# Optimization experiments

Measured on AMD Instinct MI355X. Metric: run time of the kernel, lower is better.

The kernel has to match this reference:

```python
import jax, jax.numpy as jnp
import numpy as np

N_NODES = 100000
N_EDGES = 1600000
IN_C, HID, OUT_C = 16, 64, 1


def setup_inputs() -> dict:
    key = jax.random.key(0)
    ks = jax.random.split(key, 12)
    x = jax.random.normal(ks[0], (N_NODES, IN_C), dtype=jnp.float32)
    edge_index = jax.random.randint(ks[1], (2, N_EDGES), 0, N_NODES, dtype=jnp.int32)

    def lin(k, fan_in, fan_out):
        s = 1.0 / np.sqrt(fan_in)
        kw, kb = jax.random.split(k)
        W = jax.random.uniform(kw, (fan_in, fan_out), jnp.float32, -s, s)
        b = jax.random.uniform(kb, (fan_out,), jnp.float32, -s, s)
        return W, b

    W0, b0 = lin(ks[2], IN_C, HID)      # node_mlps[0]
    W1, b1 = lin(ks[3], HID, HID)       # node_mlps[1]
    W2, b2 = lin(ks[4], HID, OUT_C)     # node_mlps[2]
    M0, bM0 = lin(ks[5], 2 * HID, HID)  # message_mlps[0] (only one used for num_layers=3)
    return {"x": x, "edge_index": edge_index, "W0": W0, "b0": b0,
            "W1": W1, "b1": b1, "W2": W2, "b2": b2, "M0": M0, "bM0": bM0}


def _message_passing(h, src, dst, M, bM):
    # gather -> concat -> linear -> scatter-add -> degree normalize
    msgs = jnp.concatenate([h[src], h[dst]], axis=1) @ M + bM  # [E, HID]
    agg = jax.ops.segment_sum(msgs, dst, num_segments=N_NODES)  # [N, HID]
    deg = jax.ops.segment_sum(jnp.ones((src.shape[0],), h.dtype), dst,
                              num_segments=N_NODES)
    deg = jnp.clip(deg, 1.0, None)[:, None]
    return agg / deg


def reference(x, edge_index, W0, b0, W1, b1, W2, b2, M0, bM0):
    src, dst = edge_index[0], edge_index[1]
    h = jax.nn.relu(x @ W0 + b0)                  # node_mlps[0] (dropout = eval identity)
    h = h + _message_passing(h, src, dst, M0, bM0)
    h = jax.nn.relu(h @ W1 + b1)                  # node_mlps[1]
    return h @ W2 + b2                            # node_mlps[2], [N, 1]
```

## Files before the change

### kernel.cpp

```cpp
#include <hip/hip_runtime.h>

#define HID 64
#define IN_C 16

typedef __attribute__((ext_vector_type(8))) short short8;
typedef __attribute__((ext_vector_type(4))) float f32x4;

__device__ __forceinline__ float bitsf(unsigned u) { return __uint_as_float(u); }
__device__ __forceinline__ float lanebcf(float v, int l) {
    return __int_as_float(__builtin_amdgcn_readlane(__float_as_int(v), l));
}
__device__ __forceinline__ float f4c(const float4& a, int c) {
    switch (c & 3) { case 0: return a.x; case 1: return a.y; case 2: return a.z; default: return a.w; }
}

__global__ void k_init(const float* __restrict__ M0, const float* __restrict__ W1,
                       const float* __restrict__ bM0, const float* __restrict__ b1,
                       ushort* __restrict__ WPhi, ushort* __restrict__ WPlo,
                       float* __restrict__ bias192) {
    int tid = blockIdx.x * 256 + threadIdx.x;
    if (tid >= 64 * 192) return;
    int cc = tid % 192;
    int k  = tid / 192;
    float w;
    if (cc < 64) {
        float a = 0.f;
#pragma unroll
        for (int m = 0; m < HID; ++m) a = fmaf(M0[k * HID + m], W1[m * HID + cc], a);
        w = a;
    } else if (cc < 128) {
        int c = cc - 64;
        float a = W1[k * HID + c];
#pragma unroll
        for (int m = 0; m < HID; ++m) a = fmaf(M0[(HID + k) * HID + m], W1[m * HID + c], a);
        w = a;
    } else {
        w = W1[k * HID + (cc - 128)];
    }
    unsigned wb = __float_as_uint(w);
    ushort hi = (ushort)(wb >> 16);
    float hif = __uint_as_float(wb & 0xffff0000u);
    ushort lo = (ushort)(__float_as_uint(w - hif) >> 16);
    int ct = cc >> 4, s = k >> 5, l = ((k >> 3) & 3) * 16 + (cc & 15), j = k & 7;
    int fi = ((ct * 2 + s) * 64 + l) * 8 + j;
    WPhi[fi] = hi;
    WPlo[fi] = lo;
    if (k == 0) {
        float bv;
        if (cc < 64) bv = 0.f;
        else if (cc < 128) {
            int c = cc - 64;
            float a = b1[c];
#pragma unroll
            for (int m = 0; m < HID; ++m) a = fmaf(bM0[m], W1[m * HID + c], a);
            bv = a;
        } else bv = b1[cc - 128];
        bias192[cc] = bv;
    }
}

__global__ __launch_bounds__(256) void k_pre(
    const float* __restrict__ x, const float* __restrict__ W0, const float* __restrict__ b0,
    const ushort* __restrict__ WPhi, const ushort* __restrict__ WPlo,
    const float* __restrict__ bias192,
    ushort* __restrict__ zb, float* __restrict__ PQ, float* __restrict__ Pp, int N)
{
    __shared__ ushort hhi[64 * 64];
    __shared__ ushort hlo[64 * 64];

    int tid  = threadIdx.x;
    int lane = tid & 63;
    int w    = tid >> 6;
    int n0   = blockIdx.x * 64;

    float w0c[IN_C];
#pragma unroll
    for (int k = 0; k < IN_C; ++k) w0c[k] = W0[k * HID + lane];
    float b0l = b0[lane];

    short8 Bhi[3][2], Blo[3][2];
    float bias[3];
#pragma unroll
    for (int i = 0; i < 3; ++i) {
        int ct = w * 3 + i;
#pragma unroll
        for (int s = 0; s < 2; ++s) {
            int fi = ((ct * 2 + s) * 64 + lane) * 8;
            Bhi[i][s] = *reinterpret_cast<const short8*>(WPhi + fi);
            Blo[i][s] = *reinterpret_cast<const short8*>(WPlo + fi);
        }
        bias[i] = bias192[ct * 16 + (lane & 15)];
    }

    int nx = n0 + w * 16 + (lane >> 2);
    float4 xq = make_float4(0.f, 0.f, 0.f, 0.f);
    if (nx < N) xq = *reinterpret_cast<const float4*>(x + (size_t)nx * IN_C + (lane & 3) * 4);

#pragma unroll
    for (int nn = 0; nn < 16; ++nn) {
        float acc = b0l;
#pragma unroll
        for (int k = 0; k < IN_C; ++k)
            acc = fmaf(lanebcf(f4c(xq, k & 3), 4 * nn + (k >> 2)), w0c[k], acc);
        float h = fmaxf(acc, 0.f);
        unsigned hb = __float_as_uint(h);
        ushort hi = (ushort)(hb >> 16);
        float hif = __uint_as_float(hb & 0xffff0000u);
        ushort lo = (ushort)(__float_as_uint(h - hif) >> 16);
        int nl = w * 16 + nn;
        int u  = ((lane >> 3) ^ (nl & 7));
        int off = nl * 64 + u * 8 + (lane & 7);
        hhi[off] = hi;
        hlo[off] = lo;
    }
    __syncthreads();

#pragma unroll
    for (int st = 0; st < 4; ++st) {
        int nloc = st * 16 + (lane & 15);
        short8 Ahi[2], Alo[2];
#pragma unroll
        for (int s = 0; s < 2; ++s) {
            int u = (s * 4 + (lane >> 4)) ^ (nloc & 7);
            int off = nloc * 64 + u * 8;
            Ahi[s] = *reinterpret_cast<const short8*>(hhi + off);
            Alo[s] = *reinterpret_cast<const short8*>(hlo + off);
        }
#pragma unroll
        for (int i = 0; i < 3; ++i) {
            int ct = w * 3 + i;
            f32x4 acc = {bias[i], bias[i], bias[i], bias[i]};
#pragma unroll
            for (int s = 0; s < 2; ++s) {
                acc = __builtin_amdgcn_mfma_f32_16x16x32_bf16(Ahi[s], Bhi[i][s], acc, 0, 0, 0);
                acc = __builtin_amdgcn_mfma_f32_16x16x32_bf16(Ahi[s], Blo[i][s], acc, 0, 0, 0);
                acc = __builtin_amdgcn_mfma_f32_16x16x32_bf16(Alo[s], Bhi[i][s], acc, 0, 0, 0);
                acc = __builtin_amdgcn_mfma_f32_16x16x32_bf16(Alo[s], Blo[i][s], acc, 0, 0, 0);
            }
            int ch = ct * 16 + (lane & 15);
#pragma unroll
            for (int r = 0; r < 4; ++r) {
                int n = n0 + st * 16 + (lane >> 4) * 4 + r;
                if (n >= N) continue;
                float v = acc[r];
                if (ch < 64) {
                    unsigned u = __float_as_uint(v);
                    unsigned rr = (u + 0x7fffu + ((u >> 16) & 1u)) >> 16;
                    zb[(size_t)n * HID + ch] = (ushort)rr;
                } else if (ch < 128) {
                    PQ[(size_t)n * HID + (ch - 64)] = v;
                } else {
                    Pp[(size_t)n * HID + (ch - 128)] = v;
                }
            }
        }
    }
}

__global__ __launch_bounds__(256) void k_p1hist(const int* __restrict__ ei, int* __restrict__ bhT,
                                                int E, int B1) {
    __shared__ int h[1024];
    int NB1 = gridDim.x;
    for (int i = threadIdx.x; i < B1; i += 256) h[i] = 0;
    __syncthreads();
    int CH = (E + NB1 - 1) / NB1;
    int e0 = blockIdx.x * CH;
    int e1 = min(e0 + CH, E);
    for (int e = e0 + (int)threadIdx.x; e < e1; e += 256)
        atomicAdd(&h[ei[E + e] >> 8], 1);
    __syncthreads();
    for (int i = threadIdx.x; i < B1; i += 256)
        bhT[(size_t)i * NB1 + blockIdx.x] = h[i];
}

__global__ void k_scan1(const int* __restrict__ cnt, int* __restrict__ rs,
                        int* __restrict__ bsum, int M) {
    __shared__ int lds[256];
    int t = threadIdx.x;
    int base = blockIdx.x * 4096 + t * 16;
    int v[16];
    if (base + 16 <= M) {
#pragma unroll
        for (int u = 0; u < 4; ++u) {
            int4 w = *reinterpret_cast<const int4*>(cnt + base + u * 4);
            v[u * 4 + 0] = w.x; v[u * 4 + 1] = w.y; v[u * 4 + 2] = w.z; v[u * 4 + 3] = w.w;
        }
    } else {
#pragma unroll
        for (int u = 0; u < 16; ++u) v[u] = (base + u < M) ? cnt[base + u] : 0;
    }
    int run = 0;
#pragma unroll
    for (int u = 0; u < 16; ++u) { int tv = v[u]; v[u] = run; run += tv; }
    lds[t] = run;
    __syncthreads();
#pragma unroll
    for (int off = 1; off < 256; off <<= 1) {
        int xw = (t >= off) ? lds[t - off] : 0;
        __syncthreads();
        lds[t] += xw;
        __syncthreads();
    }
    int excl = lds[t] - run;
    if (t == 255) bsum[blockIdx.x] = lds[255];
#pragma unroll
    for (int u = 0; u < 16; ++u)
        if (base + u < M) rs[base + u] = excl + v[u];
}

__global__ void k_scan_add(int* __restrict__ rs, const int* __restrict__ bsum,
                           int NB, int M, int E) {
    __shared__ int lds[256];
    __shared__ int excl[256];
    int t = threadIdx.x;
    int v = (t < NB) ? bsum[t] : 0;
    lds[t] = v;
    __syncthreads();
#pragma unroll
    for (int off = 1; off < 256; off <<= 1) {
        int xw = (t >= off) ? lds[t - off] : 0;
        __syncthreads();
        lds[t] += xw;
        __syncthreads();
    }
    excl[t] = lds[t] - v;
    __syncthreads();
    int i = blockIdx.x * 256 + t;
    if (i < M) rs[i] += excl[i >> 12];
    if (i == 0) rs[M] = E;
}

__global__ __launch_bounds__(256) void k_p1scat(const int* __restrict__ ei, const int* __restrict__ off,
                                                int2* __restrict__ tmp, int E, int B1) {
    __shared__ int cur[1024];
    int NB1 = gridDim.x;
    for (int i = threadIdx.x; i < B1; i += 256)
        cur[i] = off[(size_t)i * NB1 + blockIdx.x];
    __syncthreads();
    int CH = (E + NB1 - 1) / NB1;
    int e0 = blockIdx.x * CH;
    int e1 = min(e0 + CH, E);
    for (int e = e0 + (int)threadIdx.x; e < e1; e += 256) {
        int s = ei[e];
        int d = ei[E + e];
        int pos = atomicAdd(&cur[d >> 8], 1);
        tmp[pos] = make_int2(s, d);
    }
}

__global__ __launch_bounds__(256) void k_p2(const int2* __restrict__ tmp, const int* __restrict__ off,
                                            int* __restrict__ rs, int* __restrict__ csr,
                                            int E, int N, int B1, int NB1) {
    __shared__ int h2[256];
    __shared__ int sc[256];
    __shared__ int cur[256];
    int b = blockIdx.x;
    int t = threadIdx.x;
    int bb0 = off[(size_t)b * NB1];
    int bb1 = off[(size_t)(b + 1) * NB1];

    h2[t] = 0;
    __syncthreads();
    for (int i = bb0 + t; i < bb1; i += 256)
        atomicAdd(&h2[tmp[i].y & 255], 1);
    __syncthreads();

    int v = h2[t];
    sc[t] = v;
    __syncthreads();
#pragma unroll
    for (int o = 1; o < 256; o <<= 1) {
        int xw = (t >= o) ? sc[t - o] : 0;
        __syncthreads();
        sc[t] += xw;
        __syncthreads();
    }
    int excl = sc[t] - v;

    int node = b * 256 + t;
    if (node < N) rs[node] = bb0 + excl;
    if (b == B1 - 1 && t == 0) rs[N] = E;
    cur[t] = bb0 + excl;
    __syncthreads();

    for (int i = bb0 + t; i < bb1; i += 256) {
        int2 ed = tmp[i];
        int pos = atomicAdd(&cur[ed.y & 255], 1);
        csr[pos] = ed.x;
    }
}

__global__ __launch_bounds__(256) void k_final(
    const ushort* __restrict__ zb, const float* __restrict__ PQ, const float* __restrict__ Pp,
    const int* __restrict__ rs, const int* __restrict__ csr,
    const float* __restrict__ W2, const float* __restrict__ b2,
    float* __restrict__ out, int N)
{
    int lane = threadIdx.x & 63;
    int g    = lane >> 4;
    int ql   = lane & 15;
    int oct  = ql & 7;
    int half = ql >> 3;
    int wid  = (blockIdx.x * 256 + threadIdx.x) >> 6;
    int nw   = (gridDim.x * 256) >> 6;

    int c0 = oct * 8 + half * 4;
    float4 w2v = *reinterpret_cast<const float4*>(W2 + c0);
    float b2s = b2[0];

    for (int n0 = wid * 4; n0 < N; n0 += nw * 4) {
        int ng   = n0 + g;
        bool okg = ng < N;

        int rv = okg ? rs[ng + half] : 0;
        int beg = __shfl(rv, g * 16 + 0);
        int end = __shfl(rv, g * 16 + 8);
        int deg = end - beg;
        int md = deg;
        md = max(md, __shfl_xor(md, 16));
        md = max(md, __shfl_xor(md, 32));

        float acc[8];
#pragma unroll
        for (int i = 0; i < 8; ++i) acc[i] = 0.f;

        for (int c = 0; c < md; c += 32) {
            int j0 = c + ql, j1 = c + 16 + ql;
            int ia = (j0 < deg) ? csr[beg + j0] : -1;
            int ib = (j1 < deg) ? csr[beg + j1] : -1;
#pragma unroll
            for (int tb = 0; tb < 4; ++tb) {
                if (tb > 0 && md <= c + 8 * tb) break;
                int srcs[4];
#pragma unroll
                for (int t4 = 0; t4 < 4; ++t4) {
                    int t = tb * 4 + t4;
                    int e = 2 * t + half;
                    srcs[t4] = __shfl(tb < 2 ? ia : ib, g * 16 + (e & 15));
                }
                uint4 rw[4];
#pragma unroll
                for (int t4 = 0; t4 < 4; ++t4) {
                    int s = srcs[t4] < 0 ? 0 : srcs[t4];
                    rw[t4] = *reinterpret_cast<const uint4*>(zb + (size_t)s * HID + oct * 8);
                }
#pragma unroll
                for (int t4 = 0; t4 < 4; ++t4) {
                    if (srcs[t4] >= 0) {
                        uint4 wv = rw[t4];
                        acc[0] += bitsf(wv.x << 16); acc[1] += bitsf(wv.x & 0xffff0000u);
                        acc[2] += bitsf(wv.y << 16); acc[3] += bitsf(wv.y & 0xffff0000u);
                        acc[4] += bitsf(wv.z << 16); acc[5] += bitsf(wv.z & 0xffff0000u);
                        acc[6] += bitsf(wv.w << 16); acc[7] += bitsf(wv.w & 0xffff0000u);
                    }
                }
            }
        }
#pragma unroll
        for (int i = 0; i < 8; ++i) acc[i] += __shfl_xor(acc[i], 8);

        float s0 = half ? acc[4] : acc[0];
        float s1 = half ? acc[5] : acc[1];
        float s2 = half ? acc[6] : acc[2];
        float s3 = half ? acc[7] : acc[3];

        float4 base = make_float4(0.f, 0.f, 0.f, 0.f);
        if (okg) {
            base = *reinterpret_cast<const float4*>(PQ + (size_t)ng * HID + c0);
            if (deg == 0)
                base = *reinterpret_cast<const float4*>(Pp + (size_t)ng * HID + c0);
        }
        float rcpd = (deg > 0) ? (1.f / (float)deg) : 0.f;
        float y0 = base.x + s0 * rcpd;
        float y1 = base.y + s1 * rcpd;
        float y2 = base.z + s2 * rcpd;
        float y3 = base.w + s3 * rcpd;

        float part = fmaxf(y0, 0.f) * w2v.x + fmaxf(y1, 0.f) * w2v.y +
                     fmaxf(y2, 0.f) * w2v.z + fmaxf(y3, 0.f) * w2v.w;
#pragma unroll
        for (int off = 1; off < 16; off <<= 1) part += __shfl_xor(part, off);
        if (ql == 0 && okg) out[ng] = part + b2s;
    }
}

extern "C" void kernel_launch(void* const* d_in, const int* in_sizes, int n_in,
                              void* d_out, int out_size, void* d_ws, size_t ws_size,
                              hipStream_t stream) {
    const float* x   = (const float*)d_in[0];
    const int*   ei  = (const int*)d_in[1];
    const float* W0  = (const float*)d_in[2];
    const float* b0  = (const float*)d_in[3];
    const float* W1  = (const float*)d_in[4];
    const float* b1  = (const float*)d_in[5];
    const float* W2  = (const float*)d_in[6];
    const float* b2  = (const float*)d_in[7];
    const float* M0  = (const float*)d_in[8];
    const float* bM0 = (const float*)d_in[9];

    int N = in_sizes[0] / IN_C;
    int E = in_sizes[1] / 2;
    int B1 = (N + 255) >> 8;
    int NB1 = 256;
    int M2 = B1 * NB1;
    int NB = (M2 + 4095) / 4096;

    ushort* zb     = (ushort*)d_ws;
    float*  PQ     = (float*)(zb + (size_t)N * HID);
    float*  Pp     = PQ + (size_t)N * HID;
    ushort* WPhi   = (ushort*)(Pp + (size_t)N * HID);
    ushort* WPlo   = WPhi + 12288;
    float*  bias192= (float*)(WPlo + 12288);
    int*    bhT    = (int*)(bias192 + 192);
    int*    off    = bhT + (size_t)M2;
    int*    bsum   = off + (size_t)M2 + 1;
    int*    rs     = bsum + 256;
    size_t  up     = ((size_t)(rs + N + 1) + 7) & ~(size_t)7;
    int2*   tmp    = (int2*)up;
    int*    csr    = (int*)(tmp + (size_t)E);
    float*  out    = (float*)d_out;

    int npre = (N + 63) / 64;

    k_init<<<48, 256, 0, stream>>>(M0, W1, bM0, b1, WPhi, WPlo, bias192);
    k_pre<<<npre, 256, 0, stream>>>(x, W0, b0, WPhi, WPlo, bias192, zb, PQ, Pp, N);
    k_p1hist<<<NB1, 256, 0, stream>>>(ei, bhT, E, B1);
    k_scan1<<<NB, 256, 0, stream>>>(bhT, off, bsum, M2);
    k_scan_add<<<(M2 + 255) / 256, 256, 0, stream>>>(off, bsum, NB, M2, E);
    k_p1scat<<<NB1, 256, 0, stream>>>(ei, off, tmp, E, B1);
    k_p2<<<B1, 256, 0, stream>>>(tmp, off, rs, csr, E, N, B1, NB1);
    k_final<<<2048, 256, 0, stream>>>(zb, PQ, Pp, rs, csr, W2, b2, out, N);
}
```

Baseline: 112.2 us.

## Fuse edge histogram into pre kernel, vectorize outputs, pack sort temp

Merges the edge-destination histogram kernel into the node pre-processing launch as extra blocks, which removes one launch and lets both workloads overlap. It swaps the MFMA operand order so each lane holds four consecutive channels of one node, so results are written as packed bf16x4 or float4 stores instead of scattered scalar stores. It also packs the source index and low destination byte into one 32-bit word in the two-pass sort temp buffer, halving that traffic. The packing assumes source indices fit in 24 bits.

New measurement: 101.7 us. 9.3% less time.

```diff
diff --git a/kernel.cpp b/kernel.cpp
--- a/kernel.cpp
+++ b/kernel.cpp
@@ -7,6 +7,10 @@
 typedef __attribute__((ext_vector_type(4))) float f32x4;
 
 __device__ __forceinline__ float bitsf(unsigned u) { return __uint_as_float(u); }
+__device__ __forceinline__ unsigned rne16(float f) {
+    unsigned u = __float_as_uint(f);
+    return (u + 0x7fffu + ((u >> 16) & 1u)) >> 16;
+}
 __device__ __forceinline__ float lanebcf(float v, int l) {
     return __int_as_float(__builtin_amdgcn_readlane(__float_as_int(v), l));
 }
@@ -59,37 +63,53 @@
     }
 }
 
-__global__ __launch_bounds__(256) void k_pre(
+__global__ __launch_bounds__(256) void k_pre_hist(
     const float* __restrict__ x, const float* __restrict__ W0, const float* __restrict__ b0,
     const ushort* __restrict__ WPhi, const ushort* __restrict__ WPlo,
     const float* __restrict__ bias192,
-    ushort* __restrict__ zb, float* __restrict__ PQ, float* __restrict__ Pp, int N)
+    ushort* __restrict__ zb, float* __restrict__ PQ, float* __restrict__ Pp, int N,
+    const int* __restrict__ ei, int* __restrict__ bhT, int E, int B1, int NB1)
 {
     __shared__ ushort hhi[64 * 64];
     __shared__ ushort hlo[64 * 64];
 
+    if ((int)blockIdx.x < NB1) {
+        int* h = reinterpret_cast<int*>(hhi);
+        for (int i = threadIdx.x; i < B1; i += 256) h[i] = 0;
+        __syncthreads();
+        int CH = (E + NB1 - 1) / NB1;
+        int e0 = blockIdx.x * CH;
+        int e1 = min(e0 + CH, E);
+        for (int e = e0 + (int)threadIdx.x; e < e1; e += 256)
+            atomicAdd(&h[ei[E + e] >> 8], 1);
+        __syncthreads();
+        for (int i = threadIdx.x; i < B1; i += 256)
+            bhT[(size_t)i * NB1 + blockIdx.x] = h[i];
+        return;
+    }
+
     int tid  = threadIdx.x;
     int lane = tid & 63;
     int w    = tid >> 6;
-    int n0   = blockIdx.x * 64;
+    int n0   = (blockIdx.x - NB1) * 64;
 
     float w0c[IN_C];
 #pragma unroll
     for (int k = 0; k < IN_C; ++k) w0c[k] = W0[k * HID + lane];
     float b0l = b0[lane];
 
-    short8 Bhi[3][2], Blo[3][2];
-    float bias[3];
+    short8 Whi[3][2], Wlo[3][2];
+    float4 bias4[3];
 #pragma unroll
     for (int i = 0; i < 3; ++i) {
         int ct = w * 3 + i;
 #pragma unroll
         for (int s = 0; s < 2; ++s) {
             int fi = ((ct * 2 + s) * 64 + lane) * 8;
-            Bhi[i][s] = *reinterpret_cast<const short8*>(WPhi + fi);
-            Blo[i][s] = *reinterpret_cast<const short8*>(WPlo + fi);
-        }
-        bias[i] = bias192[ct * 16 + (lane & 15)];
+            Whi[i][s] = *reinterpret_cast<const short8*>(WPhi + fi);
+            Wlo[i][s] = *reinterpret_cast<const short8*>(WPlo + fi);
+        }
+        bias4[i] = *reinterpret_cast<const float4*>(bias192 + ct * 16 + (lane >> 4) * 4);
     }
 
     int nx = n0 + w * 16 + (lane >> 2);
@@ -126,51 +146,35 @@
             Ahi[s] = *reinterpret_cast<const short8*>(hhi + off);
             Alo[s] = *reinterpret_cast<const short8*>(hlo + off);
         }
+        int n = n0 + st * 16 + (lane & 15);
 #pragma unroll
         for (int i = 0; i < 3; ++i) {
             int ct = w * 3 + i;
-            f32x4 acc = {bias[i], bias[i], bias[i], bias[i]};
+            f32x4 acc = {bias4[i].x, bias4[i].y, bias4[i].z, bias4[i].w};
 #pragma unroll
             for (int s = 0; s < 2; ++s) {
-                acc = __builtin_amdgcn_mfma_f32_16x16x32_bf16(Ahi[s], Bhi[i][s], acc, 0, 0, 0);
-                acc = __builtin_amdgcn_mfma_f32_16x16x32_bf16(Ahi[s], Blo[i][s], acc, 0, 0, 0);
-                acc = __builtin_amdgcn_mfma_f32_16x16x32_bf16(Alo[s], Bhi[i][s], acc, 0, 0, 0);
-                acc = __builtin_amdgcn_mfma_f32_16x16x32_bf16(Alo[s], Blo[i][s], acc, 0, 0, 0);
+                acc = __builtin_amdgcn_mfma_f32_16x16x32_bf16(Whi[i][s], Ahi[s], acc, 0, 0, 0);
+                acc = __builtin_amdgcn_mfma_f32_16x16x32_bf16(Whi[i][s], Alo[s], acc, 0, 0, 0);
+                acc = __builtin_amdgcn_mfma_f32_16x16x32_bf16(Wlo[i][s], Ahi[s], acc, 0, 0, 0);
+                acc = __builtin_amdgcn_mfma_f32_16x16x32_bf16(Wlo[i][s], Alo[s], acc, 0, 0, 0);
             }
-            int ch = ct * 16 + (lane & 15);
-#pragma unroll
-            for (int r = 0; r < 4; ++r) {
-                int n = n0 + st * 16 + (lane >> 4) * 4 + r;
-                if (n >= N) continue;
-                float v = acc[r];
-                if (ch < 64) {
-                    unsigned u = __float_as_uint(v);
-                    unsigned rr = (u + 0x7fffu + ((u >> 16) & 1u)) >> 16;
-                    zb[(size_t)n * HID + ch] = (ushort)rr;
-                } else if (ch < 128) {
-                    PQ[(size_t)n * HID + (ch - 64)] = v;
+            if (n < N) {
+                int chb = ct * 16 + (lane >> 4) * 4;
+                if (chb < 64) {
+                    uint2 pk;
+                    pk.x = rne16(acc[0]) | (rne16(acc[1]) << 16);
+                    pk.y = rne16(acc[2]) | (rne16(acc[3]) << 16);
+                    *reinterpret_cast<uint2*>(zb + (size_t)n * HID + chb) = pk;
+                } else if (chb < 128) {
+                    float4 v = make_float4(acc[0], acc[1], acc[2], acc[3]);
+                    *reinterpret_cast<float4*>(PQ + (size_t)n * HID + (chb - 64)) = v;
                 } else {
-                    Pp[(size_t)n * HID + (ch - 128)] = v;
+                    float4 v = make_float4(acc[0], acc[1], acc[2], acc[3]);
+                    *reinterpret_cast<float4*>(Pp + (size_t)n * HID + (chb - 128)) = v;
                 }
             }
         }
     }
-}
-
-__global__ __launch_bounds__(256) void k_p1hist(const int* __restrict__ ei, int* __restrict__ bhT,
-                                                int E, int B1) {
-    __shared__ int h[1024];
-    int NB1 = gridDim.x;
-    for (int i = threadIdx.x; i < B1; i += 256) h[i] = 0;
-    __syncthreads();
-    int CH = (E + NB1 - 1) / NB1;
-    int e0 = blockIdx.x * CH;
-    int e1 = min(e0 + CH, E);
-    for (int e = e0 + (int)threadIdx.x; e < e1; e += 256)
-        atomicAdd(&h[ei[E + e] >> 8], 1);
-    __syncthreads();
-    for (int i = threadIdx.x; i < B1; i += 256)
-        bhT[(size_t)i * NB1 + blockIdx.x] = h[i];
 }
 
 __global__ void k_scan1(const int* __restrict__ cnt, int* __restrict__ rs,
@@ -231,7 +235,7 @@
 }
 
 __global__ __launch_bounds__(256) void k_p1scat(const int* __restrict__ ei, const int* __restrict__ off,
-                                                int2* __restrict__ tmp, int E, int B1) {
+                                                unsigned* __restrict__ tmp, int E, int B1) {
     __shared__ int cur[1024];
     int NB1 = gridDim.x;
     for (int i = threadIdx.x; i < B1; i += 256)
@@ -244,11 +248,11 @@
         int s = ei[e];
         int d = ei[E + e];
         int pos = atomicAdd(&cur[d >> 8], 1);
-        tmp[pos] = make_int2(s, d);
-    }
-}
-
-__global__ __launch_bounds__(256) void k_p2(const int2* __restrict__ tmp, const int* __restrict__ off,
+        tmp[pos] = (unsigned)s | ((unsigned)(d & 255) << 24);
+    }
+}
+
+__global__ __launch_bounds__(256) void k_p2(const unsigned* __restrict__ tmp, const int* __restrict__ off,
                                             int* __restrict__ rs, int* __restrict__ csr,
                                             int E, int N, int B1, int NB1) {
     __shared__ int h2[256];
@@ -262,7 +266,7 @@
     h2[t] = 0;
     __syncthreads();
     for (int i = bb0 + t; i < bb1; i += 256)
-        atomicAdd(&h2[tmp[i].y & 255], 1);
+        atomicAdd(&h2[tmp[i] >> 24], 1);
     __syncthreads();
 
     int v = h2[t];
@@ -284,9 +288,9 @@
     __syncthreads();
 
     for (int i = bb0 + t; i < bb1; i += 256) {
-        int2 ed = tmp[i];
-        int pos = atomicAdd(&cur[ed.y & 255], 1);
-        csr[pos] = ed.x;
+        unsigned ed = tmp[i];
+        int pos = atomicAdd(&cur[ed >> 24], 1);
+        csr[pos] = (int)(ed & 0x00FFFFFFu);
     }
 }
 
@@ -405,26 +409,25 @@
     int M2 = B1 * NB1;
     int NB = (M2 + 4095) / 4096;
 
-    ushort* zb     = (ushort*)d_ws;
-    float*  PQ     = (float*)(zb + (size_t)N * HID);
-    float*  Pp     = PQ + (size_t)N * HID;
-    ushort* WPhi   = (ushort*)(Pp + (size_t)N * HID);
-    ushort* WPlo   = WPhi + 12288;
-    float*  bias192= (float*)(WPlo + 12288);
-    int*    bhT    = (int*)(bias192 + 192);
-    int*    off    = bhT + (size_t)M2;
-    int*    bsum   = off + (size_t)M2 + 1;
-    int*    rs     = bsum + 256;
-    size_t  up     = ((size_t)(rs + N + 1) + 7) & ~(size_t)7;
-    int2*   tmp    = (int2*)up;
-    int*    csr    = (int*)(tmp + (size_t)E);
-    float*  out    = (float*)d_out;
+    ushort*   zb     = (ushort*)d_ws;
+    float*    PQ     = (float*)(zb + (size_t)N * HID);
+    float*    Pp     = PQ + (size_t)N * HID;
+    ushort*   WPhi   = (ushort*)(Pp + (size_t)N * HID);
+    ushort*   WPlo   = WPhi + 12288;
+    float*    bias192= (float*)(WPlo + 12288);
+    int*      bhT    = (int*)(bias192 + 192);
+    int*      off    = bhT + (size_t)M2;
+    int*      bsum   = off + (size_t)M2 + 1;
+    int*      rs     = bsum + 256;
+    unsigned* tmp    = (unsigned*)(rs + N + 1);
+    int*      csr    = (int*)(tmp + (size_t)E);
+    float*    out    = (float*)d_out;
 
     int npre = (N + 63) / 64;
 
     k_init<<<48, 256, 0, stream>>>(M0, W1, bM0, b1, WPhi, WPlo, bias192);
-    k_pre<<<npre, 256, 0, stream>>>(x, W0, b0, WPhi, WPlo, bias192, zb, PQ, Pp, N);
-    k_p1hist<<<NB1, 256, 0, stream>>>(ei, bhT, E, B1);
+    k_pre_hist<<<NB1 + npre, 256, 0, stream>>>(x, W0, b0, WPhi, WPlo, bias192,
+                                               zb, PQ, Pp, N, ei, bhT, E, B1, NB1);
     k_scan1<<<NB, 256, 0, stream>>>(bhT, off, bsum, M2);
     k_scan_add<<<(M2 + 255) / 256, 256, 0, stream>>>(off, bsum, NB, M2, E);
     k_p1scat<<<NB1, 256, 0, stream>>>(ei, off, tmp, E, B1);
```
